# Performance work log

Measured on AMD Instinct MI355X. Metric: run time of the kernel, lower is better.

## Reference

```python
import jax, jax.numpy as jnp
import numpy as np


def setup_inputs() -> dict:
    key = jax.random.key(0)
    k1, k2 = jax.random.split(key)
    B, L, D = 8, 4096, 1024
    hidden_states = jax.random.normal(k1, (B, L, D), dtype=jnp.float32)
    token_mask = jax.random.bernoulli(k2, 0.5, (B, L))
    return {"hidden_states": hidden_states, "token_mask": token_mask}


def reference(hidden_states, token_mask):
    """Compact hidden states at masked positions, left-packed and zero-padded.

    Returns (chunked: (B, M, D), counts: (B,)) where M = max tokens per row.
    Vectorized: prefix-sum over the mask gives per-row scatter destinations;
    masked-out positions are routed to a scratch slot M that is sliced off.
    """
    B, L, D = hidden_states.shape
    counts = token_mask.sum(axis=1).astype(jnp.int32)  # (B,)
    M = int(jnp.max(counts))  # data-dependent pad width (eager, matches .item())
    if M == 0:
        return hidden_states[:, :0, :], counts
    # destination index within each row: 0..count-1 for kept tokens, M for dropped
    dest = jnp.where(token_mask, jnp.cumsum(token_mask, axis=1) - 1, M)  # (B, L)
    b_idx = jnp.arange(B)[:, None]  # (B, 1)
    out = jnp.zeros((B, M + 1, D), hidden_states.dtype)
    out = out.at[b_idx, dest].set(hidden_states)  # single fused scatter
    chunked = out[:, :M, :]  # drop scratch slot
    return chunked, counts
```

## Files before the change

### kernel.cpp

```cpp
#include <hip/hip_runtime.h>
#include <hip/hip_bf16.h>


__global__ __launch_bounds__(1024) void scan_kernel(
        const int* __restrict__ mask,
        int* __restrict__ src_idx,
        int* __restrict__ counts_ws,
        float* __restrict__ counts_out,
        int L, int M) {
    const int b = blockIdx.x;
    const int t = threadIdx.x;
    const int lane = t & 63;
    const int wid  = t >> 6;
    const int base = t * 4;

    const int4 v = *(const int4*)(mask + (size_t)b * L + base);
    const int m0 = (v.x != 0), m1 = (v.y != 0), m2 = (v.z != 0), m3 = (v.w != 0);
    const int s = m0 + m1 + m2 + m3;

    int incl = s;
    #pragma unroll
    for (int off = 1; off < 64; off <<= 1) {
        int up = __shfl_up(incl, off, 64);
        if (lane >= off) incl += up;
    }

    __shared__ int wsum[16];
    __shared__ int wexc[17];
    if (lane == 63) wsum[wid] = incl;
    __syncthreads();
    if (t == 0) {
        int acc = 0;
        #pragma unroll
        for (int w = 0; w < 16; ++w) { wexc[w] = acc; acc += wsum[w]; }
        wexc[16] = acc;
        counts_ws[b] = acc;
        counts_out[b] = (float)acc;
    }
    __syncthreads();

    int prefix = wexc[wid] + (incl - s);

    int* srow = src_idx + (size_t)b * M;
    if (m0) srow[prefix++] = base + 0;
    if (m1) srow[prefix++] = base + 1;
    if (m2) srow[prefix++] = base + 2;
    if (m3) srow[prefix]   = base + 3;
}

__global__ __launch_bounds__(256) void pack_kernel(
        const float4* __restrict__ hidden,
        const int* __restrict__ src_idx,
        const int* __restrict__ counts,
        float4* __restrict__ out,
        int L, int M, int D4, int nrows) {
    const int t = threadIdx.x;
    for (int r = blockIdx.x; r < nrows; r += gridDim.x) {
        const int b = r / M;
        const int m = r - b * M;
        const size_t orow = (size_t)r * D4;
        if (m < counts[b]) {
            const int l = src_idx[r];
            const size_t irow = ((size_t)b * L + l) * D4;
            for (int i = t; i < D4; i += blockDim.x)
                out[orow + i] = hidden[irow + i];
        } else {
            const float4 z = make_float4(0.f, 0.f, 0.f, 0.f);
            for (int i = t; i < D4; i += blockDim.x)
                out[orow + i] = z;
        }
    }
}

extern "C" void kernel_launch(void* const* d_in, const int* in_sizes, int n_in,
                              void* d_out, int out_size, void* d_ws, size_t ws_size,
                              hipStream_t stream) {
    const int B = 8;
    const int BL = in_sizes[1];
    const int D  = in_sizes[0] / BL;
    const int L  = BL / B;
    const int M  = (out_size - B) / (B * D);

    const float* hidden = (const float*)d_in[0];
    const int*   mask   = (const int*)d_in[1];
    float*       out    = (float*)d_out;

    int* counts_ws = (int*)d_ws;
    int* src_idx   = (int*)d_ws + 64;

    float* counts_out = out + (size_t)B * M * D;

    scan_kernel<<<B, 1024, 0, stream>>>(mask, src_idx, counts_ws, counts_out, L, M);

    if (M > 0) {
        const int nrows = B * M;
        int grid = nrows < 2048 ? nrows : 2048;
        pack_kernel<<<grid, 256, 0, stream>>>((const float4*)hidden, src_idx,
                                              counts_ws, (float4*)out, L, M,
                                              D / 4, nrows);
    }
}
```

Baseline: 203.7 us.

## Fuse mask scan and row packing into one kernel with redundant per-block scans

Replaces the two-kernel flow (one scan kernel writing source indices to workspace, then a pack kernel) with one kernel launched as B*256 blocks. Each block rescans the whole mask row itself to find its 16-token segment's output offset, then copies that segment's kept rows and zero-fills its share of the padding rows. This removes a launch, the serialised single-block-per-batch scan, and the workspace round trip. In exchange every block repeats the full-row mask read and scan, and the work per block varies with segment density. The code hardcodes L=4096 (256 segments of 16 tokens) and D4=256 matching blockDim, and drops the M==0 counts write.

```diff
diff --git a/kernel.cpp b/kernel.cpp
--- a/kernel.cpp
+++ b/kernel.cpp
@@ -2,21 +2,31 @@
 #include <hip/hip_bf16.h>
 
 
-__global__ __launch_bounds__(1024) void scan_kernel(
+__global__ __launch_bounds__(256) void fused_pack_kernel(
+        const float4* __restrict__ hidden,
         const int* __restrict__ mask,
-        int* __restrict__ src_idx,
-        int* __restrict__ counts_ws,
+        float4* __restrict__ out,
         float* __restrict__ counts_out,
-        int L, int M) {
-    const int b = blockIdx.x;
-    const int t = threadIdx.x;
+        int L, int M, int D4) {
+    const int b   = blockIdx.x >> 8;
+    const int seg = blockIdx.x & 255;
+    const int t    = threadIdx.x;
     const int lane = t & 63;
     const int wid  = t >> 6;
-    const int base = t * 4;
 
-    const int4 v = *(const int4*)(mask + (size_t)b * L + base);
-    const int m0 = (v.x != 0), m1 = (v.y != 0), m2 = (v.z != 0), m3 = (v.w != 0);
-    const int s = m0 + m1 + m2 + m3;
+    const int* mrow = mask + (size_t)b * L;
+    const int4 v0 = *(const int4*)(mrow + t * 16 + 0);
+    const int4 v1 = *(const int4*)(mrow + t * 16 + 4);
+    const int4 v2 = *(const int4*)(mrow + t * 16 + 8);
+    const int4 v3 = *(const int4*)(mrow + t * 16 + 12);
+    int mm[16];
+    mm[0]=(v0.x!=0); mm[1]=(v0.y!=0); mm[2]=(v0.z!=0); mm[3]=(v0.w!=0);
+    mm[4]=(v1.x!=0); mm[5]=(v1.y!=0); mm[6]=(v1.z!=0); mm[7]=(v1.w!=0);
+    mm[8]=(v2.x!=0); mm[9]=(v2.y!=0); mm[10]=(v2.z!=0); mm[11]=(v2.w!=0);
+    mm[12]=(v3.x!=0); mm[13]=(v3.y!=0); mm[14]=(v3.z!=0); mm[15]=(v3.w!=0);
+    int s = 0;
+    #pragma unroll
+    for (int i = 0; i < 16; ++i) s += mm[i];
 
     int incl = s;
     #pragma unroll
@@ -25,51 +35,52 @@
         if (lane >= off) incl += up;
     }
 
-    __shared__ int wsum[16];
-    __shared__ int wexc[17];
+    __shared__ int wsum[4];
+    __shared__ int woff[4];
+    __shared__ int sh_total;
+    __shared__ int sh_base;
+    __shared__ int sh_n;
+    __shared__ int sh_src[16];
+
     if (lane == 63) wsum[wid] = incl;
     __syncthreads();
     if (t == 0) {
         int acc = 0;
         #pragma unroll
-        for (int w = 0; w < 16; ++w) { wexc[w] = acc; acc += wsum[w]; }
-        wexc[16] = acc;
-        counts_ws[b] = acc;
-        counts_out[b] = (float)acc;
+        for (int w = 0; w < 4; ++w) { woff[w] = acc; acc += wsum[w]; }
+        sh_total = acc;
     }
     __syncthreads();
 
-    int prefix = wexc[wid] + (incl - s);
+    const int exc = woff[wid] + (incl - s);
 
-    int* srow = src_idx + (size_t)b * M;
-    if (m0) srow[prefix++] = base + 0;
-    if (m1) srow[prefix++] = base + 1;
-    if (m2) srow[prefix++] = base + 2;
-    if (m3) srow[prefix]   = base + 3;
-}
+    if (t == seg) {
+        sh_base = exc;
+        int n = 0;
+        #pragma unroll
+        for (int i = 0; i < 16; ++i)
+            if (mm[i]) sh_src[n++] = seg * 16 + i;
+        sh_n = n;
+    }
+    __syncthreads();
 
-__global__ __launch_bounds__(256) void pack_kernel(
-        const float4* __restrict__ hidden,
-        const int* __restrict__ src_idx,
-        const int* __restrict__ counts,
-        float4* __restrict__ out,
-        int L, int M, int D4, int nrows) {
-    const int t = threadIdx.x;
-    for (int r = blockIdx.x; r < nrows; r += gridDim.x) {
-        const int b = r / M;
-        const int m = r - b * M;
-        const size_t orow = (size_t)r * D4;
-        if (m < counts[b]) {
-            const int l = src_idx[r];
-            const size_t irow = ((size_t)b * L + l) * D4;
-            for (int i = t; i < D4; i += blockDim.x)
-                out[orow + i] = hidden[irow + i];
-        } else {
-            const float4 z = make_float4(0.f, 0.f, 0.f, 0.f);
-            for (int i = t; i < D4; i += blockDim.x)
-                out[orow + i] = z;
-        }
+    const int n = sh_n;
+    const int base = sh_base;
+    const size_t hrow0 = (size_t)b * L;
+    const size_t orow0 = (size_t)b * M;
+    for (int j = 0; j < n; ++j) {
+        const size_t irow = (hrow0 + sh_src[j]) * D4 + t;
+        const size_t orow = (orow0 + base + j) * D4 + t;
+        out[orow] = hidden[irow];
     }
+
+    const int total = sh_total;
+    const float4 z = make_float4(0.f, 0.f, 0.f, 0.f);
+    for (int m = total + seg; m < M; m += 256) {
+        out[(orow0 + m) * D4 + t] = z;
+    }
+
+    if (seg == 0 && t == 0) counts_out[b] = (float)total;
 }
 
 extern "C" void kernel_launch(void* const* d_in, const int* in_sizes, int n_in,
@@ -84,19 +95,10 @@
     const float* hidden = (const float*)d_in[0];
     const int*   mask   = (const int*)d_in[1];
     float*       out    = (float*)d_out;
-
-    int* counts_ws = (int*)d_ws;
-    int* src_idx   = (int*)d_ws + 64;
-
     float* counts_out = out + (size_t)B * M * D;
 
-    scan_kernel<<<B, 1024, 0, stream>>>(mask, src_idx, counts_ws, counts_out, L, M);
-
     if (M > 0) {
-        const int nrows = B * M;
-        int grid = nrows < 2048 ? nrows : 2048;
-        pack_kernel<<<grid, 256, 0, stream>>>((const float4*)hidden, src_idx,
-                                              counts_ws, (float4*)out, L, M,
-                                              D / 4, nrows);
+        fused_pack_kernel<<<B * 256, 256, 0, stream>>>(
+            (const float4*)hidden, mask, (float4*)out, counts_out, L, M, D / 4);
     }
 }
```

After: 204.4 us. About the same (+0.3%).
